# Kernel tuning notes

Hardware: AMD Instinct MI355X
Metric: run time of the kernel (lower is better)

The kernel has to match this reference:

```python
import jax, jax.numpy as jnp
import numpy as np

HIDDEN = 2048
HEADS = 16
HEAD_DIM = HIDDEN // HEADS

def setup_inputs() -> dict:
    key = jax.random.key(0)
    ks = jax.random.split(key, 9)
    B, S = 1, 4096
    scale = 1.0 / np.sqrt(HIDDEN)
    x = jax.random.normal(ks[0], (B, S, HIDDEN), dtype=jnp.float32)
    Wq = jax.random.normal(ks[1], (HIDDEN, HIDDEN), dtype=jnp.float32) * scale
    Wk = jax.random.normal(ks[2], (HIDDEN, HIDDEN), dtype=jnp.float32) * scale
    Wv = jax.random.normal(ks[3], (HIDDEN, HIDDEN), dtype=jnp.float32) * scale
    Wo = jax.random.normal(ks[4], (HIDDEN, HIDDEN), dtype=jnp.float32) * scale
    bq = jax.random.normal(ks[5], (HIDDEN,), dtype=jnp.float32) * 0.01
    bk = jax.random.normal(ks[6], (HIDDEN,), dtype=jnp.float32) * 0.01
    bv = jax.random.normal(ks[7], (HIDDEN,), dtype=jnp.float32) * 0.01
    bo = jax.random.normal(ks[8], (HIDDEN,), dtype=jnp.float32) * 0.01
    return {"x": x, "Wq": Wq, "bq": bq, "Wk": Wk, "bk": bk, "Wv": Wv, "bv": bv, "Wo": Wo, "bo": bo}

def reference(x, Wq, bq, Wk, bk, Wv, bv, Wo, bo):
    B, S, D = x.shape
    H, Hd = HEADS, HEAD_DIM
    # projections (nn.Linear: x @ W^T + b)
    Q = (x @ Wq.T + bq).reshape(B, S, H, Hd).transpose(0, 2, 1, 3)  # [B,H,S,Hd]
    K = (x @ Wk.T + bk).reshape(B, S, H, Hd).transpose(0, 2, 1, 3)
    V = (x @ Wv.T + bv).reshape(B, S, H, Hd).transpose(0, 2, 1, 3)
    scores = jnp.einsum('bhqd,bhkd->bhqk', Q, K) / jnp.sqrt(jnp.float32(Hd))
    attn = jax.nn.softmax(scores, axis=-1)
    out = jnp.einsum('bhqk,bhkd->bhqd', attn, V)  # [B,H,S,Hd]
    out = out.transpose(0, 2, 1, 3).reshape(B, S, D)
    return out @ Wo.T + bo
```

## Files before the change

kernel.cpp:

```cpp
#include <hip/hip_runtime.h>

#define S_LEN  4096
#define DMODEL 2048
#define NHEADS 16
#define HDIM   128

typedef __bf16 bf16x8 __attribute__((ext_vector_type(8)));
typedef __bf16 bf16x2 __attribute__((ext_vector_type(2)));
typedef float  f32x4  __attribute__((ext_vector_type(4)));
typedef float  f32x16 __attribute__((ext_vector_type(16)));

__device__ __forceinline__ unsigned short f2b(float f) {
    unsigned int u = __float_as_uint(f);
    unsigned int r = (u + 0x7fffu + ((u >> 16) & 1u)) >> 16;
    return (unsigned short)r;
}

__device__ __forceinline__ unsigned int pkbf16(float a, float b) {
#if __has_builtin(__builtin_amdgcn_cvt_pk_bf16_f32)
    bf16x2 t = __builtin_amdgcn_cvt_pk_bf16_f32(a, b);
    return *(unsigned int*)&t;
#else
    return (unsigned int)f2b(a) | ((unsigned int)f2b(b) << 16);
#endif
}

__device__ __forceinline__ f32x4 mfma16(bf16x8 a, bf16x8 b, f32x4 c) {
    return __builtin_amdgcn_mfma_f32_16x16x32_bf16(a, b, c, 0, 0, 0);
}

__device__ __forceinline__ f32x16 mfma32(bf16x8 a, bf16x8 b, f32x16 c) {
    return __builtin_amdgcn_mfma_f32_32x32x16_bf16(a, b, c, 0, 0, 0);
}

__device__ __forceinline__ void ldg2lds16(const void* g, void* l) {
    __builtin_amdgcn_global_load_lds(
        (__attribute__((address_space(1))) void*)(void*)g,
        (__attribute__((address_space(3))) void*)l, 16, 0, 0);
}

__global__ __launch_bounds__(256) void cvt_bf16(
    const float* __restrict__ src, unsigned short* __restrict__ dst, int n4)
{
    int i = blockIdx.x * blockDim.x + threadIdx.x;
    if (i < n4) {
        float4 v = ((const float4*)src)[i];
        uint2 h;
        h.x = pkbf16(v.x, v.y); h.y = pkbf16(v.z, v.w);
        ((uint2*)dst)[i] = h;
    }
}

__global__ __launch_bounds__(256) void cvt_bf16_w4(
    const float* __restrict__ w0, const float* __restrict__ w1,
    const float* __restrict__ w2, const float* __restrict__ w3,
    unsigned short* __restrict__ d0, unsigned short* __restrict__ d1,
    unsigned short* __restrict__ d2, unsigned short* __restrict__ d3)
{
    const int z = blockIdx.y;
    const float* src = (z == 0) ? w0 : (z == 1) ? w1 : (z == 2) ? w2 : w3;
    unsigned short* dst = (z == 0) ? d0 : (z == 1) ? d1 : (z == 2) ? d2 : d3;
    int i = blockIdx.x * blockDim.x + threadIdx.x;
    float4 v = ((const float4*)src)[i];
    uint2 h;
    h.x = pkbf16(v.x, v.y); h.y = pkbf16(v.z, v.w);
    ((uint2*)dst)[i] = h;
}

__global__ __launch_bounds__(256, 2) void gemm_qkv(
    const unsigned short* __restrict__ xb,
    const unsigned short* __restrict__ Wqb, const float* __restrict__ bq,
    const unsigned short* __restrict__ Wkb, const float* __restrict__ bk,
    const unsigned short* __restrict__ Wvb, const float* __restrict__ bv,
    unsigned short* __restrict__ Qb, unsigned short* __restrict__ Kb,
    unsigned short* __restrict__ Vb)
{
    const int z = blockIdx.z;
    const unsigned short* B = (z == 0) ? Wqb : (z == 1) ? Wkb : Wvb;
    const float* bias        = (z == 0) ? bq  : (z == 1) ? bk  : bv;
    unsigned short* C        = (z == 0) ? Qb  : (z == 1) ? Kb  : Vb;
    const float oscale = (z == 0) ? 0.12751743f : 1.0f;

    __shared__ alignas(16) unsigned short As[128 * 32];
    __shared__ alignas(16) unsigned short Bs[128 * 32];

    const int tid = threadIdx.x;
    const int m0 = blockIdx.y * 128, n0 = blockIdx.x * 128;
    const int w = tid >> 6, lane = tid & 63, lo = lane & 15, qd = lane >> 4;
    const int wm = (w >> 1) * 64, wn = (w & 1) * 64;
    const int rsel = lane >> 2, csel = (lane & 3) * 8;

    f32x4 acc[4][4] = {};

    for (int k0 = 0; k0 < DMODEL; k0 += 32) {
#pragma unroll
        for (int i = 0; i < 2; i++) {
            int c = w * 2 + i;
            ldg2lds16(&xb[(size_t)(m0 + c * 16 + rsel) * DMODEL + k0 + csel],
                      &As[c * 512]);
            ldg2lds16(&B [(size_t)(n0 + c * 16 + rsel) * DMODEL + k0 + csel],
                      &Bs[c * 512]);
        }
        __syncthreads();

        bf16x8 af[4], bfr[4];
#pragma unroll
        for (int i = 0; i < 4; i++)
            af[i] = *(const bf16x8*)&As[(wm + i * 16 + lo) * 32 + qd * 8];
#pragma unroll
        for (int j = 0; j < 4; j++)
            bfr[j] = *(const bf16x8*)&Bs[(wn + j * 16 + lo) * 32 + qd * 8];
#pragma unroll
        for (int i = 0; i < 4; i++)
#pragma unroll
            for (int j = 0; j < 4; j++)
                acc[i][j] = mfma16(af[i], bfr[j], acc[i][j]);
        __syncthreads();
    }

#pragma unroll
    for (int j = 0; j < 4; j++) {
        int n = n0 + wn + j * 16 + lo;
        float bv_ = bias[n];
#pragma unroll
        for (int i = 0; i < 4; i++) {
#pragma unroll
            for (int r = 0; r < 4; r++) {
                int m = m0 + wm + i * 16 + qd * 4 + r;
                C[(size_t)m * DMODEL + n] = f2b((acc[i][j][r] + bv_) * oscale);
            }
        }
    }
}

__global__ __launch_bounds__(256, 2) void gemm_out(
    const unsigned short* __restrict__ Aatt, const unsigned short* __restrict__ Wob,
    const float* __restrict__ bo, float* __restrict__ out)
{
    __shared__ alignas(16) unsigned short As[128 * 32];
    __shared__ alignas(16) unsigned short Bs[128 * 32];

    const int tid = threadIdx.x;
    const int m0 = blockIdx.y * 128, n0 = blockIdx.x * 128;
    const int w = tid >> 6, lane = tid & 63, lo = lane & 15, qd = lane >> 4;
    const int wm = (w >> 1) * 64, wn = (w & 1) * 64;
    const int rsel = lane >> 2, csel = (lane & 3) * 8;

    f32x4 acc[4][4] = {};

    for (int k0 = 0; k0 < DMODEL; k0 += 32) {
#pragma unroll
        for (int i = 0; i < 2; i++) {
            int c = w * 2 + i;
            ldg2lds16(&Aatt[(size_t)(m0 + c * 16 + rsel) * DMODEL + k0 + csel],
                      &As[c * 512]);
            ldg2lds16(&Wob [(size_t)(n0 + c * 16 + rsel) * DMODEL + k0 + csel],
                      &Bs[c * 512]);
        }
        __syncthreads();

        bf16x8 af[4], bfr[4];
#pragma unroll
        for (int i = 0; i < 4; i++)
            af[i] = *(const bf16x8*)&As[(wm + i * 16 + lo) * 32 + qd * 8];
#pragma unroll
        for (int j = 0; j < 4; j++)
            bfr[j] = *(const bf16x8*)&Bs[(wn + j * 16 + lo) * 32 + qd * 8];
#pragma unroll
        for (int i = 0; i < 4; i++)
#pragma unroll
            for (int j = 0; j < 4; j++)
                acc[i][j] = mfma16(af[i], bfr[j], acc[i][j]);
        __syncthreads();
    }

#pragma unroll
    for (int j = 0; j < 4; j++) {
        int n = n0 + wn + j * 16 + lo;
        float bv_ = bo[n];
#pragma unroll
        for (int i = 0; i < 4; i++) {
#pragma unroll
            for (int r = 0; r < 4; r++) {
                int m = m0 + wm + i * 16 + qd * 4 + r;
                out[(size_t)m * DMODEL + n] = acc[i][j][r] + bv_;
            }
        }
    }
}

__global__ __launch_bounds__(256) void transpose_v(
    const unsigned short* __restrict__ Vb, unsigned short* __restrict__ Vt)
{
    __shared__ unsigned short tile[64 * 67];
    const int s0 = blockIdx.x * 64;
    const int d0 = blockIdx.y * 64;
    const int tid = threadIdx.x;
#pragma unroll
    for (int i = 0; i < 2; i++) {
        int chunk = tid + i * 256;
        int r = chunk >> 3, c8 = (chunk & 7) * 8;
        uint4 v = *(const uint4*)&Vb[(size_t)(s0 + r) * DMODEL + d0 + c8];
        const unsigned short* p = (const unsigned short*)&v;
#pragma unroll
        for (int j = 0; j < 8; j++) tile[r * 67 + c8 + j] = p[j];
    }
    __syncthreads();
#pragma unroll
    for (int i = 0; i < 2; i++) {
        int chunk = tid + i * 256;
        int r = chunk >> 3, c8 = (chunk & 7) * 8;
        unsigned short tmp[8];
#pragma unroll
        for (int j = 0; j < 8; j++) tmp[j] = tile[(c8 + j) * 67 + r];
        *(uint4*)&Vt[(size_t)(d0 + r) * S_LEN + s0 + c8] = *(uint4*)tmp;
    }
}

__global__ __launch_bounds__(256, 2) void attn_kernel(
    const unsigned short* __restrict__ Qb, const unsigned short* __restrict__ Kb,
    const unsigned short* __restrict__ Vt, unsigned short* __restrict__ Ob)
{
    const int id = blockIdx.x;
    const int xcd = id & 7, slot = id >> 3;
    const int h  = (xcd << 1) | (slot >> 6);
    const int q0 = (slot & 63) * 64;

    __shared__ alignas(16) unsigned char smem[66048];
    unsigned short* Ks0  = (unsigned short*)smem;
    unsigned short* Vts0 = (unsigned short*)(smem + 16384);
    unsigned short* Ks1  = (unsigned short*)(smem + 32768);
    unsigned short* Vts1 = (unsigned short*)(smem + 49152);
    float* Of = (float*)smem;
    float* Lf = (float*)(smem + 65536);

    const int tid = threadIdx.x;
    const int w = tid >> 6, lane = tid & 63;
    const int qw = w >> 1, kw = w & 1;
    const int l31 = lane & 31, hi = lane >> 5;
    const int sw7 = l31 & 7;

    bf16x8 qf[8];
    {
        const unsigned short* qrow =
            &Qb[(size_t)(q0 + qw * 32 + l31) * DMODEL + h * HDIM];
#pragma unroll
        for (int sl = 0; sl < 8; sl++)
            qf[sl] = *(const bf16x8*)&qrow[sl * 16 + hi * 8];
    }

    f32x16 o_acc[4] = {};
    float l_run = 0.f;

    const int krow = kw * 32 + l31;

#define STAGE_K(dst_, key0_)                                                  \
    {                                                                         \
        _Pragma("unroll")                                                     \
        for (int i = 0; i < 4; i++) {                                         \
            int r = w * 16 + i * 4 + (lane >> 4);                             \
            int c = (lane & 15) ^ (r & 7);                                    \
            ldg2lds16(&Kb[(size_t)((key0_) + r) * DMODEL + h * HDIM + c * 8], \
                      &(dst_)[(w * 16 + i * 4) * 128]);                       \
        }                                                                     \
    }
#define STAGE_V(dst_, key0_)                                                  \
    {                                                                         \
        _Pragma("unroll")                                                     \
        for (int i = 0; i < 4; i++) {                                         \
            int r = w * 32 + i * 8 + (lane >> 3);                             \
            int c = (lane & 7) ^ (r & 7);                                     \
            ldg2lds16(&Vt[(size_t)(h * HDIM + r) * S_LEN + (key0_) + c * 8],  \
                      &(dst_)[(w * 32 + i * 8) * 64]);                        \
        }                                                                     \
    }

#define ATTN_ITER(KsC, VtsC, KsN, VtsN, kbn)                                  \
    {                                                                         \
        if ((kbn) < S_LEN / 64) {                                             \
            STAGE_K(KsN, (kbn) * 64);                                         \
            STAGE_V(VtsN, (kbn) * 64);                                        \
        }                                                                     \
        f32x16 s = {};                                                        \
        __builtin_amdgcn_s_setprio(1);                                        \
        _Pragma("unroll")                                                     \
        for (int sl = 0; sl < 8; sl++) {                                      \
            bf16x8 kf = *(const bf16x8*)                                      \
                &(KsC)[krow * 128 + (((2 * sl + hi) ^ sw7) * 8)];             \
            s = mfma32(kf, qf[sl], s);                                        \
        }                                                                     \
        __builtin_amdgcn_s_setprio(0);                                        \
        bf16x8 pa0, pa1;                                                      \
        {                                                                     \
            float ls = 0.f;                                                   \
            _Pragma("unroll")                                                 \
            for (int k2 = 0; k2 < 2; k2++) {                                  \
                float e0 = __builtin_amdgcn_exp2f(s[8 * k2 + 0]);             \
                float e1 = __builtin_amdgcn_exp2f(s[8 * k2 + 1]);             \
                float e2 = __builtin_amdgcn_exp2f(s[8 * k2 + 2]);             \
                float e3 = __builtin_amdgcn_exp2f(s[8 * k2 + 3]);             \
                float e4 = __builtin_amdgcn_exp2f(s[8 * k2 + 4]);             \
                float e5 = __builtin_amdgcn_exp2f(s[8 * k2 + 5]);             \
                float e6 = __builtin_amdgcn_exp2f(s[8 * k2 + 6]);             \
                float e7 = __builtin_amdgcn_exp2f(s[8 * k2 + 7]);             \
                ls += ((e0 + e1) + (e2 + e3)) + ((e4 + e5) + (e6 + e7));      \
                unsigned int c0 = pkbf16(e0, e1);                             \
                unsigned int c1 = pkbf16(e2, e3);                             \
                unsigned int c2 = pkbf16(e4, e5);                             \
                unsigned int c3 = pkbf16(e6, e7);                             \
                asm("v_permlane32_swap_b32 %0, %1" : "+v"(c0), "+v"(c2));     \
                asm("v_permlane32_swap_b32 %0, %1" : "+v"(c1), "+v"(c3));     \
                uint4 u; u.x = c0; u.y = c1; u.z = c2; u.w = c3;              \
                if (k2 == 0) pa0 = *(bf16x8*)&u; else pa1 = *(bf16x8*)&u;     \
            }                                                                 \
            l_run += ls;                                                      \
        }                                                                     \
        __builtin_amdgcn_s_setprio(1);                                        \
        _Pragma("unroll")                                                     \
        for (int k2 = 0; k2 < 2; k2++) {                                      \
            const int gch = 4 * kw + 2 * k2 + hi;                             \
            bf16x8 pf = (k2 == 0) ? pa0 : pa1;                                \
            _Pragma("unroll")                                                 \
            for (int dt = 0; dt < 4; dt++) {                                  \
                bf16x8 vf = *(const bf16x8*)                                  \
                    &(VtsC)[(dt * 32 + l31) * 64 + ((gch ^ sw7) * 8)];        \
                o_acc[dt] = mfma32(pf, vf, o_acc[dt]);                        \
            }                                                                 \
        }                                                                     \
        __builtin_amdgcn_s_setprio(0);                                        \
        __syncthreads();                                                      \
    }

    STAGE_K(Ks0, 0);
    STAGE_V(Vts0, 0);
    __syncthreads();

    for (int kb = 0; kb < S_LEN / 64; kb += 2) {
        ATTN_ITER(Ks0, Vts0, Ks1, Vts1, kb + 1);
        ATTN_ITER(Ks1, Vts1, Ks0, Vts0, kb + 2);
    }
#undef ATTN_ITER
#undef STAGE_K
#undef STAGE_V

    float l = l_run + __shfl_xor(l_run, 32);

    if (kw == 1) {
#pragma unroll
        for (int dt = 0; dt < 4; dt++)
#pragma unroll
            for (int r = 0; r < 16; r++) {
                int row = (r & 3) + 8 * (r >> 2) + 4 * hi;
                Of[(qw * 32 + row) * 128 + dt * 32 + l31] = o_acc[dt][r];
            }
    }
    if (hi == 0) Lf[(qw * 2 + kw) * 32 + l31] = l;
    __syncthreads();

    if (kw == 0) {
        float linv[16];
#pragma unroll
        for (int r = 0; r < 16; r++) {
            int row = (r & 3) + 8 * (r >> 2) + 4 * hi;
            linv[r] = 1.0f / (Lf[(qw * 2 + 0) * 32 + row] +
                              Lf[(qw * 2 + 1) * 32 + row]);
        }
#pragma unroll
        for (int dt = 0; dt < 4; dt++)
#pragma unroll
            for (int r = 0; r < 16; r++) {
                int row = (r & 3) + 8 * (r >> 2) + 4 * hi;
                float v = o_acc[dt][r] + Of[(qw * 32 + row) * 128 + dt * 32 + l31];
                Ob[(size_t)(q0 + qw * 32 + row) * DMODEL + h * HDIM + dt * 32 + l31]
                    = f2b(v * linv[r]);
            }
    }
}

extern "C" void kernel_launch(void* const* d_in, const int* in_sizes, int n_in,
                              void* d_out, int out_size, void* d_ws, size_t ws_size,
                              hipStream_t stream)
{
    const float* x  = (const float*)d_in[0];
    const float* Wq = (const float*)d_in[1];
    const float* bq = (const float*)d_in[2];
    const float* Wk = (const float*)d_in[3];
    const float* bk = (const float*)d_in[4];
    const float* Wv = (const float*)d_in[5];
    const float* bv = (const float*)d_in[6];
    const float* Wo = (const float*)d_in[7];
    const float* bo = (const float*)d_in[8];
    float* out = (float*)d_out;

    const size_t N = (size_t)S_LEN * DMODEL;
    const size_t W = (size_t)DMODEL * DMODEL;
    unsigned short* Qb  = (unsigned short*)d_ws;
    unsigned short* Kb  = Qb + N;
    unsigned short* Vb  = Kb + N;
    unsigned short* xbv = Vb + N;
    unsigned short* Wqb = xbv + N;
    unsigned short* Wkb = Wqb + W;
    unsigned short* Wvb = Wkb + W;
    unsigned short* Wob = Wvb + W;
    unsigned short* Vt  = xbv;
    unsigned short* Ob  = Vb;

    cvt_bf16<<<(int)(N / 4 / 256), 256, 0, stream>>>(x, xbv, (int)(N / 4));
    cvt_bf16_w4<<<dim3((unsigned)(W / 4 / 256), 4), 256, 0, stream>>>(
        Wq, Wk, Wv, Wo, Wqb, Wkb, Wvb, Wob);

    gemm_qkv<<<dim3(DMODEL / 128, S_LEN / 128, 3), 256, 0, stream>>>(
        xbv, Wqb, bq, Wkb, bk, Wvb, bv, Qb, Kb, Vb);

    transpose_v<<<dim3(S_LEN / 64, DMODEL / 64), 256, 0, stream>>>(Vb, Vt);

    attn_kernel<<<1024, 256, 0, stream>>>(Qb, Kb, Vt, Ob);

    gemm_out<<<dim3(DMODEL / 128, S_LEN / 128), 256, 0, stream>>>(Ob, Wob, bo, out);
}
```

Measured before the change: 493.0 us.

## Pipeline projection GEMMs with triple-buffered async LDS loads and swizzled larger tiles

Both projection GEMMs move from a 128x128x32 tile with 256 threads and two full barriers per step to a 256x128x64 tile with 512 threads. Global-to-LDS loads are triple-buffered, prefetching two stages ahead under vmcnt waits, and the LDS layout uses an XOR swizzle to avoid bank conflicts. MFMA sections are wrapped in s_setprio. The goal is to hide global memory latency and cut synchronisation overhead. The cost is 144KB of LDS per block, which may limit occupancy to one block per CU.

After: 556.2 us. +12.8%, slower.

```diff
diff --git a/kernel.cpp b/kernel.cpp
--- a/kernel.cpp
+++ b/kernel.cpp
@@ -67,7 +67,75 @@
     ((uint2*)dst)[i] = h;
 }
 
-__global__ __launch_bounds__(256, 2) void gemm_qkv(
+#define GBM 256
+#define GBN 128
+#define GBK 64
+#define GNT (DMODEL / GBK)
+
+#define G_STAGE(Abase, Bbase, Amat, Bmat, kt)                                  \
+    {                                                                          \
+        const int srow = lane >> 3;                                            \
+        const int gc = (lane & 7) ^ (srow & 7);                                \
+        _Pragma("unroll")                                                      \
+        for (int j2 = 0; j2 < 4; j2++) {                                       \
+            int r = w * 32 + j2 * 8 + srow;                                    \
+            ldg2lds16(&(Amat)[(size_t)(m0 + r) * DMODEL + (kt) * GBK + gc * 8],\
+                      &(Abase)[(w * 32 + j2 * 8) * GBK]);                      \
+        }                                                                      \
+        _Pragma("unroll")                                                      \
+        for (int j2 = 0; j2 < 2; j2++) {                                       \
+            int r = w * 16 + j2 * 8 + srow;                                    \
+            ldg2lds16(&(Bmat)[(size_t)(n0 + r) * DMODEL + (kt) * GBK + gc * 8],\
+                      &(Bbase)[(w * 16 + j2 * 8) * GBK]);                      \
+        }                                                                      \
+    }
+
+#define G_COMPUTE(Abase, Bbase)                                                \
+    {                                                                          \
+        _Pragma("unroll")                                                      \
+        for (int kk = 0; kk < 2; kk++) {                                       \
+            bf16x8 af[4], bfr[4];                                              \
+            _Pragma("unroll")                                                  \
+            for (int i = 0; i < 4; i++)                                        \
+                af[i] = *(const bf16x8*)                                       \
+                    &(Abase)[(wm + i * 16 + lo) * GBK +                        \
+                             (((kk * 4 + qd) ^ (lo & 7)) * 8)];                \
+            _Pragma("unroll")                                                  \
+            for (int j = 0; j < 4; j++)                                        \
+                bfr[j] = *(const bf16x8*)                                      \
+                    &(Bbase)[(wn + j * 16 + lo) * GBK +                        \
+                             (((kk * 4 + qd) ^ (lo & 7)) * 8)];                \
+            __builtin_amdgcn_s_setprio(1);                                     \
+            _Pragma("unroll")                                                  \
+            for (int i = 0; i < 4; i++)                                        \
+                _Pragma("unroll")                                              \
+                for (int j = 0; j < 4; j++)                                    \
+                    acc[i][j] = mfma16(af[i], bfr[j], acc[i][j]);              \
+            __builtin_amdgcn_s_setprio(0);                                     \
+        }                                                                      \
+    }
+
+#define G_MAIN_LOOP(Amat, Bmat)                                                \
+    G_STAGE(sA[0], sB[0], Amat, Bmat, 0);                                      \
+    G_STAGE(sA[1], sB[1], Amat, Bmat, 1);                                      \
+    asm volatile("s_waitcnt vmcnt(6)" ::: "memory");                           \
+    __builtin_amdgcn_s_barrier();                                              \
+    {                                                                          \
+        int c = 0;                                                             \
+        for (int t = 0; t < GNT; ++t) {                                        \
+            int cn = c + 2; if (cn >= 3) cn -= 3;                              \
+            if (t + 2 < GNT) G_STAGE(sA[cn], sB[cn], Amat, Bmat, t + 2);       \
+            G_COMPUTE(sA[c], sB[c]);                                           \
+            if (t + 2 < GNT)                                                   \
+                asm volatile("s_waitcnt vmcnt(6)" ::: "memory");               \
+            else                                                               \
+                asm volatile("s_waitcnt vmcnt(0)" ::: "memory");               \
+            __builtin_amdgcn_s_barrier();                                      \
+            if (++c >= 3) c = 0;                                               \
+        }                                                                      \
+    }
+
+__global__ __launch_bounds__(512, 2) void gemm_qkv(
     const unsigned short* __restrict__ xb,
     const unsigned short* __restrict__ Wqb, const float* __restrict__ bq,
     const unsigned short* __restrict__ Wkb, const float* __restrict__ bk,
@@ -81,42 +149,22 @@
     unsigned short* C        = (z == 0) ? Qb  : (z == 1) ? Kb  : Vb;
     const float oscale = (z == 0) ? 0.12751743f : 1.0f;
 
-    __shared__ alignas(16) unsigned short As[128 * 32];
-    __shared__ alignas(16) unsigned short Bs[128 * 32];
+    __shared__ alignas(16) unsigned short smem[3 * (GBM + GBN) * GBK];
+    unsigned short* sA[3]; unsigned short* sB[3];
+#pragma unroll
+    for (int i = 0; i < 3; i++) {
+        sA[i] = smem + i * (GBM + GBN) * GBK;
+        sB[i] = sA[i] + GBM * GBK;
+    }
 
     const int tid = threadIdx.x;
-    const int m0 = blockIdx.y * 128, n0 = blockIdx.x * 128;
     const int w = tid >> 6, lane = tid & 63, lo = lane & 15, qd = lane >> 4;
     const int wm = (w >> 1) * 64, wn = (w & 1) * 64;
-    const int rsel = lane >> 2, csel = (lane & 3) * 8;
+    const int m0 = blockIdx.y * GBM, n0 = blockIdx.x * GBN;
 
     f32x4 acc[4][4] = {};
 
-    for (int k0 = 0; k0 < DMODEL; k0 += 32) {
-#pragma unroll
-        for (int i = 0; i < 2; i++) {
-            int c = w * 2 + i;
-            ldg2lds16(&xb[(size_t)(m0 + c * 16 + rsel) * DMODEL + k0 + csel],
-                      &As[c * 512]);
-            ldg2lds16(&B [(size_t)(n0 + c * 16 + rsel) * DMODEL + k0 + csel],
-                      &Bs[c * 512]);
-        }
-        __syncthreads();
-
-        bf16x8 af[4], bfr[4];
-#pragma unroll
-        for (int i = 0; i < 4; i++)
-            af[i] = *(const bf16x8*)&As[(wm + i * 16 + lo) * 32 + qd * 8];
-#pragma unroll
-        for (int j = 0; j < 4; j++)
-            bfr[j] = *(const bf16x8*)&Bs[(wn + j * 16 + lo) * 32 + qd * 8];
-#pragma unroll
-        for (int i = 0; i < 4; i++)
-#pragma unroll
-            for (int j = 0; j < 4; j++)
-                acc[i][j] = mfma16(af[i], bfr[j], acc[i][j]);
-        __syncthreads();
-    }
+    G_MAIN_LOOP(xb, B);
 
 #pragma unroll
     for (int j = 0; j < 4; j++) {
@@ -133,46 +181,26 @@
     }
 }
 
-__global__ __launch_bounds__(256, 2) void gemm_out(
+__global__ __launch_bounds__(512, 2) void gemm_out(
     const unsigned short* __restrict__ Aatt, const unsigned short* __restrict__ Wob,
     const float* __restrict__ bo, float* __restrict__ out)
 {
-    __shared__ alignas(16) unsigned short As[128 * 32];
-    __shared__ alignas(16) unsigned short Bs[128 * 32];
+    __shared__ alignas(16) unsigned short smem[3 * (GBM + GBN) * GBK];
+    unsigned short* sA[3]; unsigned short* sB[3];
+#pragma unroll
+    for (int i = 0; i < 3; i++) {
+        sA[i] = smem + i * (GBM + GBN) * GBK;
+        sB[i] = sA[i] + GBM * GBK;
+    }
 
     const int tid = threadIdx.x;
-    const int m0 = blockIdx.y * 128, n0 = blockIdx.x * 128;
     const int w = tid >> 6, lane = tid & 63, lo = lane & 15, qd = lane >> 4;
     const int wm = (w >> 1) * 64, wn = (w & 1) * 64;
-    const int rsel = lane >> 2, csel = (lane & 3) * 8;
+    const int m0 = blockIdx.y * GBM, n0 = blockIdx.x * GBN;
 
     f32x4 acc[4][4] = {};
 
-    for (int k0 = 0; k0 < DMODEL; k0 += 32) {
-#pragma unroll
-        for (int i = 0; i < 2; i++) {
-            int c = w * 2 + i;
-            ldg2lds16(&Aatt[(size_t)(m0 + c * 16 + rsel) * DMODEL + k0 + csel],
-                      &As[c * 512]);
-            ldg2lds16(&Wob [(size_t)(n0 + c * 16 + rsel) * DMODEL + k0 + csel],
-                      &Bs[c * 512]);
-        }
-        __syncthreads();
-
-        bf16x8 af[4], bfr[4];
-#pragma unroll
-        for (int i = 0; i < 4; i++)
-            af[i] = *(const bf16x8*)&As[(wm + i * 16 + lo) * 32 + qd * 8];
-#pragma unroll
-        for (int j = 0; j < 4; j++)
-            bfr[j] = *(const bf16x8*)&Bs[(wn + j * 16 + lo) * 32 + qd * 8];
-#pragma unroll
-        for (int i = 0; i < 4; i++)
-#pragma unroll
-            for (int j = 0; j < 4; j++)
-                acc[i][j] = mfma16(af[i], bfr[j], acc[i][j]);
-        __syncthreads();
-    }
+    G_MAIN_LOOP(Aatt, Wob);
 
 #pragma unroll
     for (int j = 0; j < 4; j++) {
@@ -409,12 +437,12 @@
     cvt_bf16_w4<<<dim3((unsigned)(W / 4 / 256), 4), 256, 0, stream>>>(
         Wq, Wk, Wv, Wo, Wqb, Wkb, Wvb, Wob);
 
-    gemm_qkv<<<dim3(DMODEL / 128, S_LEN / 128, 3), 256, 0, stream>>>(
+    gemm_qkv<<<dim3(DMODEL / GBN, S_LEN / GBM, 3), 512, 0, stream>>>(
         xbv, Wqb, bq, Wkb, bk, Wvb, bv, Qb, Kb, Vb);
 
     transpose_v<<<dim3(S_LEN / 64, DMODEL / 64), 256, 0, stream>>>(Vb, Vt);
 
     attn_kernel<<<1024, 256, 0, stream>>>(Qb, Kb, Vt, Ob);
 
-    gemm_out<<<dim3(DMODEL / 128, S_LEN / 128), 256, 0, stream>>>(Ob, Wob, bo, out);
-}
+    gemm_out<<<dim3(DMODEL / GBN, S_LEN / GBM), 512, 0, stream>>>(Ob, Wob, bo, out);
+}
```
